# Performance work log

Measured on AMD Instinct MI355X. Metric: run time of the kernel, lower is better.

The kernel has to match this reference:

```python
import jax, jax.numpy as jnp
import numpy as np


def gcn_conv(x, src, dst, W, b, n_nodes):
    # PyG GCNConv with self-loops and symmetric normalization.
    h = x @ W                                        # [N, out]
    deg = jax.ops.segment_sum(jnp.ones_like(dst, dtype=h.dtype), dst,
                              num_segments=n_nodes)  # includes self-loops
    dinv = jnp.where(deg > 0, jax.lax.rsqrt(deg), 0.0)
    norm = dinv[src] * dinv[dst]                     # [E]
    msg = h[src] * norm[:, None]                     # gather + scale
    out = jax.ops.segment_sum(msg, dst, num_segments=n_nodes)
    return out + b


def setup_inputs() -> dict:
    key = jax.random.key(0)
    ks = jax.random.split(key, 16)
    N, E, F_IN, H, H2, C = 150000, 2400000, 61, 32, 16, 3
    x = jax.random.normal(ks[0], (N, F_IN), dtype=jnp.float32)
    edge_index = jax.random.randint(ks[1], (2, E), 0, N, dtype=jnp.int64)

    def lin(k, fin, fout):
        kw, kb = jax.random.split(k)
        s = 1.0 / np.sqrt(fin)
        W = jax.random.uniform(kw, (fin, fout), jnp.float32, -s, s)
        b = jax.random.uniform(kb, (fout,), jnp.float32, -s, s)
        return W, b

    W1, b1 = lin(ks[2], F_IN, H)
    W2, b2 = lin(ks[3], H, H)
    W3, b3 = lin(ks[4], H, H)
    W4, b4 = lin(ks[5], H, H)
    Wl1, bl1 = lin(ks[6], H, H2)
    Wl2, bl2 = lin(ks[7], H2, C)
    return {"x": x, "edge_index": edge_index,
            "W1": W1, "b1": b1, "W2": W2, "b2": b2,
            "W3": W3, "b3": b3, "W4": W4, "b4": b4,
            "Wl1": Wl1, "bl1": bl1, "Wl2": Wl2, "bl2": bl2}


def reference(x, edge_index, W1, b1, W2, b2, W3, b3, W4, b4, Wl1, bl1, Wl2, bl2):
    n = x.shape[0]
    loops = jnp.arange(n, dtype=edge_index.dtype)
    src = jnp.concatenate([edge_index[0], loops])
    dst = jnp.concatenate([edge_index[1], loops])
    # dropout p=0.25 is identity in eval mode
    h = jax.nn.relu(gcn_conv(x, src, dst, W1, b1, n))
    h = jax.nn.relu(gcn_conv(h, src, dst, W2, b2, n))
    h = jax.nn.relu(gcn_conv(h, src, dst, W3, b3, n))
    h = jax.nn.relu(gcn_conv(h, src, dst, W4, b4, n))
    g = jnp.sum(h, axis=0)                           # sum pool over all nodes -> [32]
    g = jax.nn.relu(g @ Wl1 + bl1)
    return g @ Wl2 + bl2                             # [3]
```

## Files before the change

### kernel.cpp

```cpp
#include <hip/hip_runtime.h>
#include <hip/hip_fp16.h>

#define F_IN 61
#define H 32
#define BUCK_BITS 8
#define BUCK_SZ   256
#define CHUNK     2048
#define XPAD 72
#define CMAX 6144

typedef _Float16 f16x8 __attribute__((ext_vector_type(8)));
typedef float    f32x4 __attribute__((ext_vector_type(4)));

__global__ __launch_bounds__(256) void scan1_kernel(const int* __restrict__ in,
                                                    int* __restrict__ scanned,
                                                    int* __restrict__ btot, int n) {
    __shared__ int s[256];
    int tid = threadIdx.x;
    int i = blockIdx.x * 256 + tid;
    int v = (i < n) ? in[i] : 0;
    s[tid] = v;
    __syncthreads();
    for (int off = 1; off < 256; off <<= 1) {
        int t = (tid >= off) ? s[tid - off] : 0;
        __syncthreads();
        s[tid] += t;
        __syncthreads();
    }
    if (i < n) scanned[i] = s[tid] - v;
    if (tid == 255) btot[blockIdx.x] = s[255];
}

__global__ __launch_bounds__(1024) void scan2_kernel(int* __restrict__ btot, int nB) {
    __shared__ int s[1024];
    int tid = threadIdx.x;
    int base = tid << 2;
    int v0 = (base + 0 < nB) ? btot[base + 0] : 0;
    int v1 = (base + 1 < nB) ? btot[base + 1] : 0;
    int v2 = (base + 2 < nB) ? btot[base + 2] : 0;
    int v3 = (base + 3 < nB) ? btot[base + 3] : 0;
    int sum = v0 + v1 + v2 + v3;
    s[tid] = sum;
    __syncthreads();
    for (int off = 1; off < 1024; off <<= 1) {
        int t = (tid >= off) ? s[tid - off] : 0;
        __syncthreads();
        s[tid] += t;
        __syncthreads();
    }
    int run = s[tid] - sum;
    if (base + 0 < nB) { btot[base + 0] = run; run += v0; }
    if (base + 1 < nB) { btot[base + 1] = run; run += v1; }
    if (base + 2 < nB) { btot[base + 2] = run; run += v2; }
    if (base + 3 < nB) { btot[base + 3] = run; }
}

__global__ __launch_bounds__(256) void histA_kernel(const int* __restrict__ ei,
                                                    int* __restrict__ counts,
                                                    float* __restrict__ gs,
                                                    int E, int B, int nbuck) {
    __shared__ int h[640];
    int tid = threadIdx.x;
    if (blockIdx.x == 0) {
        #pragma unroll
        for (int r = 0; r < 8; r++) gs[r * 256 + tid] = 0.f;
    }
    for (int i = tid; i < nbuck; i += 256) h[i] = 0;
    __syncthreads();
    int e0 = blockIdx.x * CHUNK;
    int e1 = e0 + CHUNK; if (e1 > E) e1 = E;
    for (int e = e0 + tid; e < e1; e += 256)
        atomicAdd(&h[ei[E + e] >> BUCK_BITS], 1);
    __syncthreads();
    for (int i = tid; i < nbuck; i += 256) counts[i * B + blockIdx.x] = h[i];
}

__global__ __launch_bounds__(256) void binB_kernel(const int* __restrict__ ei,
                                                   const int* __restrict__ countsS,
                                                   const int* __restrict__ btot,
                                                   int* __restrict__ tmp,
                                                   int E, int B, int nbuck) {
    __shared__ int gshift[640];
    __shared__ int lhist[640];
    __shared__ int lcur[640];
    __shared__ int ebuf[CHUNK];
    __shared__ unsigned short bbuf[CHUNK];
    __shared__ int sc[256];
    int tid = threadIdx.x;
    for (int i = tid; i < 640; i += 256) lhist[i] = 0;
    int e0 = blockIdx.x * CHUNK;
    int e1 = e0 + CHUNK; if (e1 > E) e1 = E;
    int cnt = e1 - e0;
    __syncthreads();
    for (int e = e0 + tid; e < e1; e += 256)
        atomicAdd(&lhist[ei[E + e] >> BUCK_BITS], 1);
    __syncthreads();
    int carry = 0;
    for (int s0 = 0; s0 < 640; s0 += 256) {
        int idx = s0 + tid;
        int v = (idx < 640) ? lhist[idx] : 0;
        sc[tid] = v;
        __syncthreads();
        for (int off = 1; off < 256; off <<= 1) {
            int t = (tid >= off) ? sc[tid - off] : 0;
            __syncthreads();
            sc[tid] += t;
            __syncthreads();
        }
        int excl = sc[tid] - v + carry;
        if (idx < 640) {
            lcur[idx] = excl;
            if (idx < nbuck) {
                int ci = idx * B + blockIdx.x;
                gshift[idx] = (countsS[ci] + btot[ci >> 8]) - excl;
            }
        }
        carry += sc[255];
        __syncthreads();
    }
    for (int e = e0 + tid; e < e1; e += 256) {
        int s = ei[e];
        int d = ei[E + e];
        int b = d >> BUCK_BITS;
        int lp = atomicAdd(&lcur[b], 1);
        ebuf[lp] = (s << BUCK_BITS) | (d & (BUCK_SZ - 1));
        bbuf[lp] = (unsigned short)b;
    }
    __syncthreads();
    for (int j = tid; j < cnt; j += 256)
        tmp[j + gshift[bbuf[j]]] = ebuf[j];
}

__global__ __launch_bounds__(256) void binC_kernel(const int* __restrict__ countsS,
                                                   const int* __restrict__ btot,
                                                   const int* __restrict__ tmp,
                                                   int* __restrict__ src_sorted,
                                                   int* __restrict__ row_start,
                                                   float* __restrict__ dinv,
                                                   __half* __restrict__ bufA,
                                                   __half* __restrict__ bufB,
                                                   int N, int E, int B, int nbuck) {
    __shared__ int hist[BUCK_SZ];
    __shared__ int pre[BUCK_SZ];
    __shared__ int lcur[BUCK_SZ];
    __shared__ int ebuf[CMAX];
    __shared__ int obuf[CMAX];
    int tid = threadIdx.x;
    int b = blockIdx.x;
    int base = b << BUCK_BITS;
    if (b == 0 && tid < H) {
        bufA[(size_t)N * H + tid] = __float2half(0.f);
        bufB[(size_t)N * H + tid] = __float2half(0.f);
    }
    int c0 = b * B;
    int e0 = countsS[c0] + btot[c0 >> 8];
    int e1 = E;
    if (b + 1 < nbuck) {
        int c1 = (b + 1) * B;
        e1 = countsS[c1] + btot[c1 >> 8];
    }
    int cnt = e1 - e0;
    bool fits = (cnt <= CMAX);
    hist[tid] = 0;
    __syncthreads();
    if (fits) {
        for (int j = tid; j < cnt; j += 256) {
            int p = tmp[e0 + j];
            ebuf[j] = p;
            atomicAdd(&hist[p & (BUCK_SZ - 1)], 1);
        }
    } else {
        for (int j = tid; j < cnt; j += 256)
            atomicAdd(&hist[tmp[e0 + j] & (BUCK_SZ - 1)], 1);
    }
    __syncthreads();
    int v = hist[tid];
    pre[tid] = v;
    __syncthreads();
    for (int off = 1; off < 256; off <<= 1) {
        int t = (tid >= off) ? pre[tid - off] : 0;
        __syncthreads();
        pre[tid] += t;
        __syncthreads();
    }
    int excl = pre[tid] - v;
    int node = base + tid;
    if (node < N) {
        row_start[node] = e0 + excl;
        dinv[node] = rsqrtf((float)v + 1.0f);
        if (node == N - 1) row_start[N] = E;
    }
    lcur[tid] = fits ? excl : (e0 + excl);
    __syncthreads();
    if (fits) {
        for (int j = tid; j < cnt; j += 256) {
            int p = ebuf[j];
            int pos = atomicAdd(&lcur[p & (BUCK_SZ - 1)], 1);
            obuf[pos] = (p >> BUCK_BITS) << 6;
        }
        __syncthreads();
        for (int j = tid; j < cnt; j += 256)
            src_sorted[e0 + j] = obuf[j];
    } else {
        for (int j = tid; j < cnt; j += 256) {
            int p = tmp[e0 + j];
            int pos = atomicAdd(&lcur[p & (BUCK_SZ - 1)], 1);
            src_sorted[pos] = (p >> BUCK_BITS) << 6;
        }
    }
}

__global__ __launch_bounds__(256) void gemm1_kernel(const float* __restrict__ x,
                                                    const float* __restrict__ W,
                                                    const float* __restrict__ dinv,
                                                    __half* __restrict__ h, int N) {
    __shared__ _Float16 Wt[H * XPAD];
    __shared__ _Float16 xs[64 * XPAD];
    int tid = threadIdx.x;
    for (int i = tid; i < 2048; i += 256) {
        int k = i >> 5, f = i & 31;
        Wt[f * XPAD + k] = (k < F_IN) ? (_Float16)W[k * H + f] : (_Float16)0.f;
    }
    int nb = blockIdx.x * 64;
    int navail = N - nb; if (navail > 64) navail = 64;
    int lim = navail * F_IN;
    const float* xb = x + (long long)nb * F_IN;
    for (int i = tid; i < 64 * F_IN; i += 256) {
        int n = i / F_IN, k = i - n * F_IN;
        xs[n * XPAD + k] = (i < lim) ? (_Float16)xb[i] : (_Float16)0.f;
    }
    if (tid < 192) {
        int n = tid / 3, k = F_IN + (tid - n * 3);
        xs[n * XPAD + k] = (_Float16)0.f;
    }
    __syncthreads();
    int w = tid >> 6, lane = tid & 63;
    int l16 = lane & 15, g = lane >> 4;
    const f16x8* ax  = (const f16x8*)&xs[(w * 16 + l16) * XPAD + g * 8];
    const f16x8* bw0 = (const f16x8*)&Wt[l16 * XPAD + g * 8];
    const f16x8* bw1 = (const f16x8*)&Wt[(16 + l16) * XPAD + g * 8];
    f16x8 a0 = ax[0],  a1 = ax[4];
    f16x8 b00 = bw0[0], b01 = bw0[4];
    f16x8 b10 = bw1[0], b11 = bw1[4];
    f32x4 acc0 = {0.f, 0.f, 0.f, 0.f};
    f32x4 acc1 = {0.f, 0.f, 0.f, 0.f};
    acc0 = __builtin_amdgcn_mfma_f32_16x16x32_f16(a0, b00, acc0, 0, 0, 0);
    acc0 = __builtin_amdgcn_mfma_f32_16x16x32_f16(a1, b01, acc0, 0, 0, 0);
    acc1 = __builtin_amdgcn_mfma_f32_16x16x32_f16(a0, b10, acc1, 0, 0, 0);
    acc1 = __builtin_amdgcn_mfma_f32_16x16x32_f16(a1, b11, acc1, 0, 0, 0);
    int nodebase = nb + w * 16 + g * 4;
    #pragma unroll
    for (int r = 0; r < 4; r++) {
        int node = nodebase + r;
        if (node < N) {
            float di = dinv[node];
            h[(long long)node * H + l16]      = __float2half(acc0[r] * di);
            h[(long long)node * H + 16 + l16] = __float2half(acc1[r] * di);
        }
    }
}

__global__ __launch_bounds__(256) void agg_gemm_kernel(const int* __restrict__ row_start,
                                                       const int* __restrict__ src_sorted,
                                                       const float* __restrict__ dinv,
                                                       const __half* __restrict__ hs,
                                                       const float* __restrict__ b,
                                                       const float* __restrict__ Wn,
                                                       __half* __restrict__ hout, int N) {
    __shared__ float Ws[H * H];
    __shared__ float t[8 * H];
    int tid = threadIdx.x;
    for (int i = tid; i < H * H; i += 256) Ws[i] = Wn[i];
    int nl = tid >> 5;
    int lane32 = tid & 31;
    int p = lane32 >> 4;
    int fp = lane32 & 15;
    int node = blockIdx.x * 8 + nl;
    int zoff = N << 6;
    __half2 accA = __floats2half2_rn(0.f, 0.f);
    __half2 accB = __floats2half2_rn(0.f, 0.f);
    if (node < N) {
        const char* hbase = (const char*)hs + (fp << 2);
        int e0 = row_start[node], e1 = row_start[node + 1];
        int idxv = (e0 + lane32 < e1) ? src_sorted[e0 + lane32] : zoff;
        for (int base = e0; base < e1; base += 32) {
            int w = e1 - base; if (w > 32) w = 32;
            int idxN = (base + 32 + lane32 < e1) ? src_sorted[base + 32 + lane32] : zoff;
            for (int j = 0; j < w; j += 16) {
                int offs[8];
                #pragma unroll
                for (int k = 0; k < 8; k++) offs[k] = __shfl(idxv, j + 2 * k + p, 32);
                unsigned g[8];
                #pragma unroll
                for (int k = 0; k < 8; k++) g[k] = *(const unsigned*)(hbase + offs[k]);
                #pragma unroll
                for (int k = 0; k < 8; k += 2) {
                    accA = __hadd2(accA, *(__half2*)&g[k]);
                    accB = __hadd2(accB, *(__half2*)&g[k + 1]);
                }
            }
            idxv = idxN;
        }
    }
    __half2 accH = __hadd2(accA, accB);
    float2 acc = __half22float2(accH);
    acc.x += __shfl_xor(acc.x, 16, 32);
    acc.y += __shfl_xor(acc.y, 16, 32);
    if (node < N && p == 0) {
        float di = dinv[node];
        unsigned sv = *(const unsigned*)((const char*)hs + ((long long)node << 6) + (fp << 2));
        float2 s2 = __half22float2(*(__half2*)&sv);
        float2 bv = ((const float2*)b)[fp];
        float rx = fmaxf(di * (acc.x + s2.x) + bv.x, 0.f);
        float ry = fmaxf(di * (acc.y + s2.y) + bv.y, 0.f);
        ((float2*)&t[nl * H])[fp] = make_float2(rx, ry);
    }
    __syncthreads();
    if (node < N) {
        int f = lane32;
        float s = 0.f;
        #pragma unroll
        for (int k = 0; k < H; k++) s += t[nl * H + k] * Ws[k * H + f];
        hout[(long long)node * H + f] = __float2half(s * dinv[node]);
    }
}

__global__ __launch_bounds__(256) void agg_pool_kernel(const int* __restrict__ row_start,
                                                       const int* __restrict__ src_sorted,
                                                       const float* __restrict__ dinv,
                                                       const __half* __restrict__ hs,
                                                       const float* __restrict__ b,
                                                       float* __restrict__ gs, int N) {
    __shared__ float t[8 * H];
    int tid = threadIdx.x;
    int nl = tid >> 5;
    int lane32 = tid & 31;
    int p = lane32 >> 4;
    int fp = lane32 & 15;
    int node = blockIdx.x * 8 + nl;
    int zoff = N << 6;
    __half2 accA = __floats2half2_rn(0.f, 0.f);
    __half2 accB = __floats2half2_rn(0.f, 0.f);
    if (node < N) {
        const char* hbase = (const char*)hs + (fp << 2);
        int e0 = row_start[node], e1 = row_start[node + 1];
        int idxv = (e0 + lane32 < e1) ? src_sorted[e0 + lane32] : zoff;
        for (int base = e0; base < e1; base += 32) {
            int w = e1 - base; if (w > 32) w = 32;
            int idxN = (base + 32 + lane32 < e1) ? src_sorted[base + 32 + lane32] : zoff;
            for (int j = 0; j < w; j += 16) {
                int offs[8];
                #pragma unroll
                for (int k = 0; k < 8; k++) offs[k] = __shfl(idxv, j + 2 * k + p, 32);
                unsigned g[8];
                #pragma unroll
                for (int k = 0; k < 8; k++) g[k] = *(const unsigned*)(hbase + offs[k]);
                #pragma unroll
                for (int k = 0; k < 8; k += 2) {
                    accA = __hadd2(accA, *(__half2*)&g[k]);
                    accB = __hadd2(accB, *(__half2*)&g[k + 1]);
                }
            }
            idxv = idxN;
        }
    }
    __half2 accH = __hadd2(accA, accB);
    float2 acc = __half22float2(accH);
    acc.x += __shfl_xor(acc.x, 16, 32);
    acc.y += __shfl_xor(acc.y, 16, 32);
    if (p == 0) {
        float2 r = make_float2(0.f, 0.f);
        if (node < N) {
            float di = dinv[node];
            unsigned sv = *(const unsigned*)((const char*)hs + ((long long)node << 6) + (fp << 2));
            float2 s2 = __half22float2(*(__half2*)&sv);
            float2 bv = ((const float2*)b)[fp];
            r.x = fmaxf(di * (acc.x + s2.x) + bv.x, 0.f);
            r.y = fmaxf(di * (acc.y + s2.y) + bv.y, 0.f);
        }
        ((float2*)&t[nl * H])[fp] = r;
    }
    __syncthreads();
    if (tid < H) {
        float s = 0.f;
        #pragma unroll
        for (int rI = 0; rI < 8; rI++) s += t[rI * H + tid];
        atomicAdd(&gs[(blockIdx.x & 63) * H + tid], s);
    }
}

__global__ __launch_bounds__(64) void head_kernel(const float* __restrict__ gs,
                                                  const float* __restrict__ Wl1,
                                                  const float* __restrict__ bl1,
                                                  const float* __restrict__ Wl2,
                                                  const float* __restrict__ bl2,
                                                  float* __restrict__ out) {
    __shared__ float gg[H];
    __shared__ float t[16];
    int tid = threadIdx.x;
    if (tid < H) {
        float s = 0.f;
        for (int c = 0; c < 64; c++) s += gs[c * H + tid];
        gg[tid] = s;
    }
    __syncthreads();
    if (tid < 16) {
        float s = bl1[tid];
        #pragma unroll
        for (int k = 0; k < 32; k++) s += gg[k] * Wl1[k * 16 + tid];
        t[tid] = fmaxf(s, 0.f);
    }
    __syncthreads();
    if (tid < 3) {
        float s = bl2[tid];
        #pragma unroll
        for (int k = 0; k < 16; k++) s += t[k] * Wl2[k * 3 + tid];
        out[tid] = s;
    }
}

extern "C" void kernel_launch(void* const* d_in, const int* in_sizes, int n_in,
                              void* d_out, int out_size, void* d_ws, size_t ws_size,
                              hipStream_t stream) {
    const float* x   = (const float*)d_in[0];
    const int*   ei  = (const int*)d_in[1];
    const float* W1  = (const float*)d_in[2];
    const float* b1  = (const float*)d_in[3];
    const float* W2  = (const float*)d_in[4];
    const float* b2  = (const float*)d_in[5];
    const float* W3  = (const float*)d_in[6];
    const float* b3  = (const float*)d_in[7];
    const float* W4  = (const float*)d_in[8];
    const float* b4  = (const float*)d_in[9];
    const float* Wl1 = (const float*)d_in[10];
    const float* bl1 = (const float*)d_in[11];
    const float* Wl2 = (const float*)d_in[12];
    const float* bl2 = (const float*)d_in[13];
    float* out = (float*)d_out;

    const int N = in_sizes[0] / F_IN;
    const int E = in_sizes[1] / 2;
    const int nbuck = (N + BUCK_SZ - 1) >> BUCK_BITS;
    const int B = (E + CHUNK - 1) / CHUNK;
    const int nC = nbuck * B;

    char* ws = (char*)d_ws;
    size_t off = 0;
    auto alloc = [&](size_t bytes) {
        char* p = ws + off;
        off += (bytes + 255) & ~(size_t)255;
        return p;
    };
    float* dinv       = (float*)alloc((size_t)N * 4);
    int*   row_start  = (int*)alloc((size_t)(N + 1) * 4);
    int*   counts     = (int*)alloc((size_t)nC * 4);
    int*   countsS    = (int*)alloc((size_t)nC * 4);
    int*   btot2      = (int*)alloc(((size_t)nC / 256 + 2) * 4);
    int*   src_sorted = (int*)alloc((size_t)E * 4);
    int*   tmp        = (int*)alloc((size_t)E * 4);
    __half* bufA      = (__half*)alloc((size_t)(N + 1) * H * 2);
    __half* bufB      = (__half*)alloc((size_t)(N + 1) * H * 2);
    float* gs         = (float*)alloc(64 * H * 4);

    const int TB = 256;
    const int gC  = (nC + TB - 1) / TB;
    const int gN8 = (N + 7) / 8;
    const int gN64 = (N + 63) / 64;

    histA_kernel<<<B, TB, 0, stream>>>(ei, counts, gs, E, B, nbuck);
    scan1_kernel<<<gC, TB, 0, stream>>>(counts, countsS, btot2, nC);
    scan2_kernel<<<1, 1024, 0, stream>>>(btot2, gC);
    binB_kernel<<<B, TB, 0, stream>>>(ei, countsS, btot2, tmp, E, B, nbuck);
    binC_kernel<<<nbuck, TB, 0, stream>>>(countsS, btot2, tmp, src_sorted, row_start,
                                          dinv, bufA, bufB, N, E, B, nbuck);

    gemm1_kernel<<<gN64, TB, 0, stream>>>(x, W1, dinv, bufA, N);
    agg_gemm_kernel<<<gN8, TB, 0, stream>>>(row_start, src_sorted, dinv, bufA, b1, W2, bufB, N);
    agg_gemm_kernel<<<gN8, TB, 0, stream>>>(row_start, src_sorted, dinv, bufB, b2, W3, bufA, N);
    agg_gemm_kernel<<<gN8, TB, 0, stream>>>(row_start, src_sorted, dinv, bufA, b3, W4, bufB, N);
    agg_pool_kernel<<<gN8, TB, 0, stream>>>(row_start, src_sorted, dinv, bufB, b4, gs, N);

    head_kernel<<<1, 64, 0, stream>>>(gs, Wl1, bl1, Wl2, bl2, out);
}
```

Baseline: 354.3 us.

## Store intermediate node features as FP8 to halve gather traffic

Hidden node features between GCN layers are stored as 8-bit FP8 (32 bytes per node) instead of FP16, and the aggregation kernels gather 4-byte words holding four features each, decode them with hardware FP8-to-float conversion and accumulate in fp32. Source indices are rescaled to the new row stride. This is meant to halve the bytes moved by the random neighbour gathers that dominate the layers. The cost is much lower feature precision, which may push the pooled output outside tolerance.

```diff
diff --git a/kernel.cpp b/kernel.cpp
--- a/kernel.cpp
+++ b/kernel.cpp
@@ -8,9 +8,15 @@
 #define CHUNK     2048
 #define XPAD 72
 #define CMAX 6144
+#define RB 32
 
 typedef _Float16 f16x8 __attribute__((ext_vector_type(8)));
 typedef float    f32x4 __attribute__((ext_vector_type(4)));
+typedef float    f32x2 __attribute__((ext_vector_type(2)));
+
+static __device__ __forceinline__ unsigned char f32_to_fp8(float v) {
+    return (unsigned char)(__builtin_amdgcn_cvt_pk_fp8_f32(v, v, 0, false) & 0xFF);
+}
 
 __global__ __launch_bounds__(256) void scan1_kernel(const int* __restrict__ in,
                                                     int* __restrict__ scanned,
@@ -137,8 +143,8 @@
                                                    int* __restrict__ src_sorted,
                                                    int* __restrict__ row_start,
                                                    float* __restrict__ dinv,
-                                                   __half* __restrict__ bufA,
-                                                   __half* __restrict__ bufB,
+                                                   unsigned char* __restrict__ bufA,
+                                                   unsigned char* __restrict__ bufB,
                                                    int N, int E, int B, int nbuck) {
     __shared__ int hist[BUCK_SZ];
     __shared__ int pre[BUCK_SZ];
@@ -148,9 +154,9 @@
     int tid = threadIdx.x;
     int b = blockIdx.x;
     int base = b << BUCK_BITS;
-    if (b == 0 && tid < H) {
-        bufA[(size_t)N * H + tid] = __float2half(0.f);
-        bufB[(size_t)N * H + tid] = __float2half(0.f);
+    if (b == 0 && tid < 8) {
+        ((unsigned int*)(bufA + ((size_t)N << 5)))[tid] = 0u;
+        ((unsigned int*)(bufB + ((size_t)N << 5)))[tid] = 0u;
     }
     int c0 = b * B;
     int e0 = countsS[c0] + btot[c0 >> 8];
@@ -196,7 +202,7 @@
         for (int j = tid; j < cnt; j += 256) {
             int p = ebuf[j];
             int pos = atomicAdd(&lcur[p & (BUCK_SZ - 1)], 1);
-            obuf[pos] = (p >> BUCK_BITS) << 6;
+            obuf[pos] = (p >> BUCK_BITS) << 5;
         }
         __syncthreads();
         for (int j = tid; j < cnt; j += 256)
@@ -205,7 +211,7 @@
         for (int j = tid; j < cnt; j += 256) {
             int p = tmp[e0 + j];
             int pos = atomicAdd(&lcur[p & (BUCK_SZ - 1)], 1);
-            src_sorted[pos] = (p >> BUCK_BITS) << 6;
+            src_sorted[pos] = (p >> BUCK_BITS) << 5;
         }
     }
 }
@@ -213,7 +219,7 @@
 __global__ __launch_bounds__(256) void gemm1_kernel(const float* __restrict__ x,
                                                     const float* __restrict__ W,
                                                     const float* __restrict__ dinv,
-                                                    __half* __restrict__ h, int N) {
+                                                    unsigned char* __restrict__ h, int N) {
     __shared__ _Float16 Wt[H * XPAD];
     __shared__ _Float16 xs[64 * XPAD];
     int tid = threadIdx.x;
@@ -254,8 +260,8 @@
         int node = nodebase + r;
         if (node < N) {
             float di = dinv[node];
-            h[(long long)node * H + l16]      = __float2half(acc0[r] * di);
-            h[(long long)node * H + 16 + l16] = __float2half(acc1[r] * di);
+            h[((long long)node << 5) + l16]      = f32_to_fp8(acc0[r] * di);
+            h[((long long)node << 5) + 16 + l16] = f32_to_fp8(acc1[r] * di);
         }
     }
 }
@@ -263,57 +269,61 @@
 __global__ __launch_bounds__(256) void agg_gemm_kernel(const int* __restrict__ row_start,
                                                        const int* __restrict__ src_sorted,
                                                        const float* __restrict__ dinv,
-                                                       const __half* __restrict__ hs,
+                                                       const unsigned char* __restrict__ hs,
                                                        const float* __restrict__ b,
                                                        const float* __restrict__ Wn,
-                                                       __half* __restrict__ hout, int N) {
+                                                       unsigned char* __restrict__ hout, int N) {
     __shared__ float Ws[H * H];
     __shared__ float t[8 * H];
     int tid = threadIdx.x;
     for (int i = tid; i < H * H; i += 256) Ws[i] = Wn[i];
     int nl = tid >> 5;
     int lane32 = tid & 31;
-    int p = lane32 >> 4;
-    int fp = lane32 & 15;
+    int slot = lane32 >> 3;
+    int fq = lane32 & 7;
     int node = blockIdx.x * 8 + nl;
-    int zoff = N << 6;
-    __half2 accA = __floats2half2_rn(0.f, 0.f);
-    __half2 accB = __floats2half2_rn(0.f, 0.f);
+    int zoff = N << 5;
+    float a0 = 0.f, a1 = 0.f, a2 = 0.f, a3 = 0.f;
     if (node < N) {
-        const char* hbase = (const char*)hs + (fp << 2);
+        const char* hbase = (const char*)hs + (fq << 2);
         int e0 = row_start[node], e1 = row_start[node + 1];
         int idxv = (e0 + lane32 < e1) ? src_sorted[e0 + lane32] : zoff;
         for (int base = e0; base < e1; base += 32) {
             int w = e1 - base; if (w > 32) w = 32;
             int idxN = (base + 32 + lane32 < e1) ? src_sorted[base + 32 + lane32] : zoff;
             for (int j = 0; j < w; j += 16) {
-                int offs[8];
-                #pragma unroll
-                for (int k = 0; k < 8; k++) offs[k] = __shfl(idxv, j + 2 * k + p, 32);
-                unsigned g[8];
-                #pragma unroll
-                for (int k = 0; k < 8; k++) g[k] = *(const unsigned*)(hbase + offs[k]);
-                #pragma unroll
-                for (int k = 0; k < 8; k += 2) {
-                    accA = __hadd2(accA, *(__half2*)&g[k]);
-                    accB = __hadd2(accB, *(__half2*)&g[k + 1]);
+                int offs[4];
+                #pragma unroll
+                for (int k = 0; k < 4; k++) offs[k] = __shfl(idxv, j + (k << 2) + slot, 32);
+                unsigned g[4];
+                #pragma unroll
+                for (int k = 0; k < 4; k++) g[k] = *(const unsigned*)(hbase + offs[k]);
+                #pragma unroll
+                for (int k = 0; k < 4; k++) {
+                    f32x2 lo = __builtin_amdgcn_cvt_pk_f32_fp8((int)g[k], false);
+                    f32x2 hi = __builtin_amdgcn_cvt_pk_f32_fp8((int)g[k], true);
+                    a0 += lo.x; a1 += lo.y; a2 += hi.x; a3 += hi.y;
                 }
             }
             idxv = idxN;
         }
     }
-    __half2 accH = __hadd2(accA, accB);
-    float2 acc = __half22float2(accH);
-    acc.x += __shfl_xor(acc.x, 16, 32);
-    acc.y += __shfl_xor(acc.y, 16, 32);
-    if (node < N && p == 0) {
+    a0 += __shfl_xor(a0, 8, 32);  a1 += __shfl_xor(a1, 8, 32);
+    a2 += __shfl_xor(a2, 8, 32);  a3 += __shfl_xor(a3, 8, 32);
+    a0 += __shfl_xor(a0, 16, 32); a1 += __shfl_xor(a1, 16, 32);
+    a2 += __shfl_xor(a2, 16, 32); a3 += __shfl_xor(a3, 16, 32);
+    if (node < N && lane32 < 8) {
         float di = dinv[node];
-        unsigned sv = *(const unsigned*)((const char*)hs + ((long long)node << 6) + (fp << 2));
-        float2 s2 = __half22float2(*(__half2*)&sv);
-        float2 bv = ((const float2*)b)[fp];
-        float rx = fmaxf(di * (acc.x + s2.x) + bv.x, 0.f);
-        float ry = fmaxf(di * (acc.y + s2.y) + bv.y, 0.f);
-        ((float2*)&t[nl * H])[fp] = make_float2(rx, ry);
+        unsigned sv = *(const unsigned*)(hs + ((long long)node << 5) + (fq << 2));
+        f32x2 slo = __builtin_amdgcn_cvt_pk_f32_fp8((int)sv, false);
+        f32x2 shi = __builtin_amdgcn_cvt_pk_f32_fp8((int)sv, true);
+        float4 bv = ((const float4*)b)[fq];
+        float4 r;
+        r.x = fmaxf(di * (a0 + slo.x) + bv.x, 0.f);
+        r.y = fmaxf(di * (a1 + slo.y) + bv.y, 0.f);
+        r.z = fmaxf(di * (a2 + shi.x) + bv.z, 0.f);
+        r.w = fmaxf(di * (a3 + shi.y) + bv.w, 0.f);
+        ((float4*)&t[nl * H])[fq] = r;
     }
     __syncthreads();
     if (node < N) {
@@ -321,64 +331,67 @@
         float s = 0.f;
         #pragma unroll
         for (int k = 0; k < H; k++) s += t[nl * H + k] * Ws[k * H + f];
-        hout[(long long)node * H + f] = __float2half(s * dinv[node]);
+        hout[((long long)node << 5) + f] = f32_to_fp8(s * dinv[node]);
     }
 }
 
 __global__ __launch_bounds__(256) void agg_pool_kernel(const int* __restrict__ row_start,
                                                        const int* __restrict__ src_sorted,
                                                        const float* __restrict__ dinv,
-                                                       const __half* __restrict__ hs,
+                                                       const unsigned char* __restrict__ hs,
                                                        const float* __restrict__ b,
                                                        float* __restrict__ gs, int N) {
     __shared__ float t[8 * H];
     int tid = threadIdx.x;
     int nl = tid >> 5;
     int lane32 = tid & 31;
-    int p = lane32 >> 4;
-    int fp = lane32 & 15;
+    int slot = lane32 >> 3;
+    int fq = lane32 & 7;
     int node = blockIdx.x * 8 + nl;
-    int zoff = N << 6;
-    __half2 accA = __floats2half2_rn(0.f, 0.f);
-    __half2 accB = __floats2half2_rn(0.f, 0.f);
+    int zoff = N << 5;
+    float a0 = 0.f, a1 = 0.f, a2 = 0.f, a3 = 0.f;
     if (node < N) {
-        const char* hbase = (const char*)hs + (fp << 2);
+        const char* hbase = (const char*)hs + (fq << 2);
         int e0 = row_start[node], e1 = row_start[node + 1];
         int idxv = (e0 + lane32 < e1) ? src_sorted[e0 + lane32] : zoff;
         for (int base = e0; base < e1; base += 32) {
             int w = e1 - base; if (w > 32) w = 32;
             int idxN = (base + 32 + lane32 < e1) ? src_sorted[base + 32 + lane32] : zoff;
             for (int j = 0; j < w; j += 16) {
-                int offs[8];
-                #pragma unroll
-                for (int k = 0; k < 8; k++) offs[k] = __shfl(idxv, j + 2 * k + p, 32);
-                unsigned g[8];
-                #pragma unroll
-                for (int k = 0; k < 8; k++) g[k] = *(const unsigned*)(hbase + offs[k]);
-                #pragma unroll
-                for (int k = 0; k < 8; k += 2) {
-                    accA = __hadd2(accA, *(__half2*)&g[k]);
-                    accB = __hadd2(accB, *(__half2*)&g[k + 1]);
+                int offs[4];
+                #pragma unroll
+                for (int k = 0; k < 4; k++) offs[k] = __shfl(idxv, j + (k << 2) + slot, 32);
+                unsigned g[4];
+                #pragma unroll
+                for (int k = 0; k < 4; k++) g[k] = *(const unsigned*)(hbase + offs[k]);
+                #pragma unroll
+                for (int k = 0; k < 4; k++) {
+                    f32x2 lo = __builtin_amdgcn_cvt_pk_f32_fp8((int)g[k], false);
+                    f32x2 hi = __builtin_amdgcn_cvt_pk_f32_fp8((int)g[k], true);
+                    a0 += lo.x; a1 += lo.y; a2 += hi.x; a3 += hi.y;
                 }
             }
             idxv = idxN;
         }
     }
-    __half2 accH = __hadd2(accA, accB);
-    float2 acc = __half22float2(accH);
-    acc.x += __shfl_xor(acc.x, 16, 32);
-    acc.y += __shfl_xor(acc.y, 16, 32);
-    if (p == 0) {
-        float2 r = make_float2(0.f, 0.f);
+    a0 += __shfl_xor(a0, 8, 32);  a1 += __shfl_xor(a1, 8, 32);
+    a2 += __shfl_xor(a2, 8, 32);  a3 += __shfl_xor(a3, 8, 32);
+    a0 += __shfl_xor(a0, 16, 32); a1 += __shfl_xor(a1, 16, 32);
+    a2 += __shfl_xor(a2, 16, 32); a3 += __shfl_xor(a3, 16, 32);
+    if (lane32 < 8) {
+        float4 r = make_float4(0.f, 0.f, 0.f, 0.f);
         if (node < N) {
             float di = dinv[node];
-            unsigned sv = *(const unsigned*)((const char*)hs + ((long long)node << 6) + (fp << 2));
-            float2 s2 = __half22float2(*(__half2*)&sv);
-            float2 bv = ((const float2*)b)[fp];
-            r.x = fmaxf(di * (acc.x + s2.x) + bv.x, 0.f);
-            r.y = fmaxf(di * (acc.y + s2.y) + bv.y, 0.f);
-        }
-        ((float2*)&t[nl * H])[fp] = r;
+            unsigned sv = *(const unsigned*)(hs + ((long long)node << 5) + (fq << 2));
+            f32x2 slo = __builtin_amdgcn_cvt_pk_f32_fp8((int)sv, false);
+            f32x2 shi = __builtin_amdgcn_cvt_pk_f32_fp8((int)sv, true);
+            float4 bv = ((const float4*)b)[fq];
+            r.x = fmaxf(di * (a0 + slo.x) + bv.x, 0.f);
+            r.y = fmaxf(di * (a1 + slo.y) + bv.y, 0.f);
+            r.z = fmaxf(di * (a2 + shi.x) + bv.z, 0.f);
+            r.w = fmaxf(di * (a3 + shi.y) + bv.w, 0.f);
+        }
+        ((float4*)&t[nl * H])[fq] = r;
     }
     __syncthreads();
     if (tid < H) {
@@ -458,8 +471,8 @@
     int*   btot2      = (int*)alloc(((size_t)nC / 256 + 2) * 4);
     int*   src_sorted = (int*)alloc((size_t)E * 4);
     int*   tmp        = (int*)alloc((size_t)E * 4);
-    __half* bufA      = (__half*)alloc((size_t)(N + 1) * H * 2);
-    __half* bufB      = (__half*)alloc((size_t)(N + 1) * H * 2);
+    unsigned char* bufA = (unsigned char*)alloc((size_t)(N + 1) * RB);
+    unsigned char* bufB = (unsigned char*)alloc((size_t)(N + 1) * RB);
     float* gs         = (float*)alloc(64 * H * 4);
 
     const int TB = 256;
```

Measured after the change: 343.3 us. 1.03x faster.
